# Kernel tuning notes

Hardware: AMD Instinct MI355X
Metric: run time of the kernel (lower is better)

## Reference

```python
import jax, jax.numpy as jnp
import numpy as np

N, E, B, DIM, NF, EF, HID = 50000, 100000, 2000, 64, 14, 4, 128


def setup_inputs() -> dict:
    key = jax.random.key(0)
    ks = jax.random.split(key, 30)
    rn = lambda k, shape, scale: jax.random.normal(k, shape, jnp.float32) * scale
    inp = {}
    inp["x"] = rn(ks[0], (N, NF), 1.0)
    inp["edge_attr"] = jax.random.uniform(ks[1], (E, EF), jnp.float32)
    inp["edge_index"] = jax.random.randint(ks[2], (2, E), 0, N)
    # equal-size graphs: 25 nodes per graph, sorted segment ids
    inp["batch"] = (jnp.arange(N, dtype=jnp.int32) // (N // B)).astype(jnp.int32)
    inp["lin0_w"] = rn(ks[3], (DIM, NF), (1.0 / NF) ** 0.5)
    inp["lin0_b"] = jnp.zeros((DIM,), jnp.float32)
    inp["mlp_w1"] = rn(ks[4], (HID, EF), (1.0 / EF) ** 0.5)
    inp["mlp_b1"] = jnp.zeros((HID,), jnp.float32)
    inp["mlp_w2"] = rn(ks[5], (DIM * DIM, HID), (1.0 / HID) ** 0.5)
    inp["mlp_b2"] = jnp.zeros((DIM * DIM,), jnp.float32)
    inp["root"] = rn(ks[6], (DIM, DIM), (1.0 / DIM) ** 0.5)
    inp["conv_b"] = jnp.zeros((DIM,), jnp.float32)
    inp["gru_wih"] = rn(ks[7], (3 * DIM, DIM), (1.0 / DIM) ** 0.5)
    inp["gru_whh"] = rn(ks[8], (3 * DIM, DIM), (1.0 / DIM) ** 0.5)
    inp["gru_bih"] = jnp.zeros((3 * DIM,), jnp.float32)
    inp["gru_bhh"] = jnp.zeros((3 * DIM,), jnp.float32)
    inp["lstm_wih"] = rn(ks[9], (4 * DIM, 2 * DIM), (1.0 / (2 * DIM)) ** 0.5)
    inp["lstm_whh"] = rn(ks[10], (4 * DIM, DIM), (1.0 / DIM) ** 0.5)
    inp["lstm_bih"] = jnp.zeros((4 * DIM,), jnp.float32)
    inp["lstm_bhh"] = jnp.zeros((4 * DIM,), jnp.float32)
    inp["lin1_w"] = rn(ks[11], (DIM, 2 * DIM), (1.0 / (2 * DIM)) ** 0.5)
    inp["lin1_b"] = jnp.zeros((DIM,), jnp.float32)
    inp["lin2_w"] = rn(ks[12], (1, DIM), (1.0 / DIM) ** 0.5)
    inp["lin2_b"] = jnp.zeros((1,), jnp.float32)
    return inp


def _forward(x, edge_attr, edge_index, batch, lin0_w, lin0_b, mlp_w1, mlp_b1,
             mlp_w2, mlp_b2, root, conv_b, gru_wih, gru_whh, gru_bih, gru_bhh,
             lstm_wih, lstm_whh, lstm_bih, lstm_bhh, lin1_w, lin1_b, lin2_w, lin2_b):
    src, dst = edge_index[0], edge_index[1]
    n = x.shape[0]
    # edge MLP -> per-edge weight matrices [E, DIM, DIM]
    h_e = jax.nn.relu(edge_attr @ mlp_w1.T + mlp_b1)
    W_e = (h_e @ mlp_w2.T + mlp_b2).reshape(-1, DIM, DIM)
    deg = jnp.clip(jax.ops.segment_sum(jnp.ones_like(dst, jnp.float32), dst, n), 1.0)

    out = jax.nn.relu(x @ lin0_w.T + lin0_b)
    h = out  # GRU hidden (seq_len=1, 1 layer)
    for _ in range(3):
        msg = jnp.einsum('ei,eio->eo', out[src], W_e)  # per-edge matmul
        agg = jax.ops.segment_sum(msg, dst, n) / deg[:, None]  # scatter-mean
        m = jax.nn.relu(agg + out @ root + conv_b)  # NNConv: aggr + root + bias
        # GRU step
        gi = m @ gru_wih.T + gru_bih
        gh = h @ gru_whh.T + gru_bhh
        i_r, i_z, i_n = jnp.split(gi, 3, axis=-1)
        h_r, h_z, h_n = jnp.split(gh, 3, axis=-1)
        r = jax.nn.sigmoid(i_r + h_r)
        z = jax.nn.sigmoid(i_z + h_z)
        ng = jnp.tanh(i_n + r * h_n)
        h = (1.0 - z) * ng + z * h
        out = h

    # Set2Set pooling, 3 processing steps
    b = B
    qh = jnp.zeros((b, DIM), out.dtype)
    qc = jnp.zeros((b, DIM), out.dtype)
    q_star = jnp.zeros((b, 2 * DIM), out.dtype)
    for _ in range(3):
        gates = q_star @ lstm_wih.T + lstm_bih + qh @ lstm_whh.T + lstm_bhh
        gi_, gf_, gg_, go_ = jnp.split(gates, 4, axis=-1)
        qc = jax.nn.sigmoid(gf_) * qc + jax.nn.sigmoid(gi_) * jnp.tanh(gg_)
        qh = jax.nn.sigmoid(go_) * jnp.tanh(qc)
        q = qh
        e = jnp.sum(out * q[batch], axis=-1)  # [N]
        e_max = jax.ops.segment_max(e, batch, b)
        a = jnp.exp(e - e_max[batch])
        denom = jax.ops.segment_sum(a, batch, b)
        a = a / denom[batch]
        r_read = jax.ops.segment_sum(a[:, None] * out, batch, b)
        q_star = jnp.concatenate([q, r_read], axis=-1)

    y = jax.nn.relu(q_star @ lin1_w.T + lin1_b)
    y = y @ lin2_w.T + lin2_b
    return y.reshape(-1)


def reference(x, edge_attr, edge_index, batch, lin0_w, lin0_b, mlp_w1, mlp_b1,
              mlp_w2, mlp_b2, root, conv_b, gru_wih, gru_whh, gru_bih, gru_bhh,
              lstm_wih, lstm_whh, lstm_bih, lstm_bhh, lin1_w, lin1_b, lin2_w, lin2_b):
    return _forward(x, edge_attr, edge_index, batch, lin0_w, lin0_b, mlp_w1, mlp_b1,
                    mlp_w2, mlp_b2, root, conv_b, gru_wih, gru_whh, gru_bih, gru_bhh,
                    lstm_wih, lstm_whh, lstm_bih, lstm_bhh, lin1_w, lin1_b, lin2_w, lin2_b)
```

## Files before the change

### kernel.cpp

```cpp
#include <hip/hip_runtime.h>
#include <hip/hip_bf16.h>

#define NN 50000
#define EE 100000
#define BB 2000
#define DIM 64
#define NF 14
#define EF 4
#define HID 128
#define EPAD 100096
#define EPAD2 100352

typedef __attribute__((ext_vector_type(8))) _Float16 half8;
typedef __attribute__((ext_vector_type(4))) _Float16 half4;
typedef __attribute__((ext_vector_type(4))) float floatx4;

__device__ __forceinline__ float rcp_fast(float x) { return __builtin_amdgcn_rcpf(x); }
__device__ __forceinline__ float sig_fast(float x) { return rcp_fast(1.f + __expf(-x)); }
__device__ __forceinline__ float tanh_fast(float x) {
    float e = __expf(2.f * x);
    return 1.f - 2.f * rcp_fast(e + 1.f);
}

__global__ void prep_fused_kernel(
    const float* __restrict__ x, const float* __restrict__ lin0_w,
    const float* __restrict__ lin0_b, float* __restrict__ hv,
    const float* __restrict__ ea, const float* __restrict__ w1,
    const float* __restrict__ b1, _Float16* __restrict__ he,
    const int* __restrict__ ei, float* __restrict__ deg,
    const float* __restrict__ w2, _Float16* __restrict__ W2rT,
    const float* __restrict__ lih, const float* __restrict__ lhh,
    const float* __restrict__ l1, float* __restrict__ lihT,
    float* __restrict__ lhhT, float* __restrict__ l1T,
    const float* __restrict__ root, const float* __restrict__ b2,
    const float* __restrict__ gwih, const float* __restrict__ gwhh,
    const float* __restrict__ gbih, const float* __restrict__ gbhh,
    _Float16* __restrict__ W1h, _Float16* __restrict__ W2h,
    float* __restrict__ fbias) {
    int t = blockIdx.x * 256 + threadIdx.x;

    {
        int el = t >> 4, hc = t & 15;
        if (el < EPAD2) {
            half8 o8 = {0, 0, 0, 0, 0, 0, 0, 0};
            if (el < EE) {
                const float4 a = *(const float4*)(ea + (size_t)el * 4);
                #pragma unroll
                for (int j = 0; j < 8; j++) {
                    int h = hc * 8 + j;
                    const float4 w = *(const float4*)(w1 + h * 4);
                    float acc = fmaxf(b1[h] + a.x * w.x + a.y * w.y + a.z * w.z + a.w * w.w, 0.f);
                    o8[j] = (_Float16)acc;
                }
                if (hc == 0) atomicAdd(&deg[ei[EE + el]], 1.0f);
            }
            *(half8*)(he + (size_t)el * 128 + hc * 8) = o8;
        }
    }
    if (t < NN * 8) {
        int n = t >> 3, dc = t & 7;
        float xv[NF];
        #pragma unroll
        for (int f = 0; f < NF; f++) xv[f] = x[(size_t)n * NF + f];
        float o[8];
        #pragma unroll
        for (int j = 0; j < 8; j++) {
            int d = dc * 8 + j;
            float acc = lin0_b[d];
            #pragma unroll
            for (int f = 0; f < NF; f++) acc += xv[f] * lin0_w[d * NF + f];
            o[j] = fmaxf(acc, 0.f);
        }
        *(float4*)(hv + (size_t)n * 64 + dc * 8)     = make_float4(o[0], o[1], o[2], o[3]);
        *(float4*)(hv + (size_t)n * 64 + dc * 8 + 4) = make_float4(o[4], o[5], o[6], o[7]);
    }
    if (t < 64 * 1024) {
        int o = t >> 10, kc = t & 1023;
        int k0 = kc * 8, i = k0 >> 7, h0 = k0 & 127;
        const float* src = w2 + (size_t)(i * 64 + o) * 128 + h0;
        const float4 a = *(const float4*)src;
        const float4 b = *(const float4*)(src + 4);
        half8 r = {(_Float16)a.x, (_Float16)a.y, (_Float16)a.z, (_Float16)a.w,
                   (_Float16)b.x, (_Float16)b.y, (_Float16)b.z, (_Float16)b.w};
        *(half8*)(W2rT + (size_t)o * 8192 + k0) = r;
    }
    if (t < 256 * 128) { int j = t / 128, k = t % 128; lihT[k * 256 + j] = lih[t]; }
    if (t < 256 * 64) { int j = t / 64, k = t % 64; lhhT[k * 256 + j] = lhh[t]; }
    if (t < 64 * 128) { int d = t / 128, k = t % 128; l1T[k * 64 + d] = l1[t]; }
    if (t < 64 * 128) {
        int n = t >> 7, k = t & 127;
        W1h[t] = (_Float16)(k < 64 ? root[k * 64 + n] : b2[(size_t)(k - 64) * 64 + n]);
    }
    if (t < 256 * 128) {
        int n2 = t >> 7, k = t & 127;
        int g = n2 >> 6, j = n2 & 63;
        float v;
        if (g == 0)      v = (k < 64) ? gwih[j * 64 + k]         : gwhh[j * 64 + (k - 64)];
        else if (g == 1) v = (k < 64) ? gwih[(64 + j) * 64 + k]  : gwhh[(64 + j) * 64 + (k - 64)];
        else if (g == 2) v = (k < 64) ? gwih[(128 + j) * 64 + k] : 0.f;
        else             v = (k < 64) ? 0.f                      : gwhh[(128 + j) * 64 + (k - 64)];
        W2h[t] = (_Float16)v;
    }
    if (t < 256) {
        int g = t >> 6, j = t & 63;
        float v = (g == 0) ? gbih[j] + gbhh[j]
                : (g == 1) ? gbih[64 + j] + gbhh[64 + j]
                : (g == 2) ? gbih[128 + j] : gbhh[128 + j];
        fbias[t] = v;
    }
}

__global__ __launch_bounds__(256, 2) void msg_gemm_kernel(
    const float* __restrict__ hv, const _Float16* __restrict__ he16,
    const _Float16* __restrict__ W2rT, const int* __restrict__ ei,
    float* __restrict__ agg, float* __restrict__ xsum) {
    __shared__ _Float16 sB[2][16 * 64 * 8];
    __shared__ _Float16 sXs[256 * 68];
    __shared__ int sDst[256];
    const int t = threadIdx.x;
    const int eb = blockIdx.x * 256;
    const int lane = t & 63;
    const int w = t >> 6;
    const int col = lane & 15;
    const int quad = lane >> 4;

    if (t < 256) {
        int e = eb + t;
        sDst[t] = (e < EE) ? ei[EE + e] : 0;
    }
    #pragma unroll 4
    for (int rep = 0; rep < 16; rep++) {
        int idx = rep * 256 + t;
        int el = idx >> 4, d4 = idx & 15;
        int e = eb + el;
        float4 v = {0.f, 0.f, 0.f, 0.f};
        if (e < EE) {
            int src = ei[e];
            v = *(const float4*)(hv + (size_t)src * 64 + d4 * 4);
        }
        half4 h4 = {(_Float16)v.x, (_Float16)v.y, (_Float16)v.z, (_Float16)v.w};
        *(half4*)&sXs[el * 68 + d4 * 4] = h4;
    }

    half8 heReg[4][4];
    #pragma unroll
    for (int mt = 0; mt < 4; mt++) {
        int row = eb + w * 64 + mt * 16 + col;
        #pragma unroll
        for (int p = 0; p < 4; p++)
            heReg[mt][p] = *(const half8*)(he16 + (size_t)row * 128 + p * 32 + quad * 8);
    }

    floatx4 Cacc[4][4];
    #pragma unroll
    for (int mt = 0; mt < 4; mt++)
        #pragma unroll
        for (int nt = 0; nt < 4; nt++)
            Cacc[mt][nt] = (floatx4){0.f, 0.f, 0.f, 0.f};

    const size_t gbase = (size_t)(w * 16 + col) * 8192 + quad * 8;
    half8 pre[4];
    {
        #pragma unroll
        for (int rep = 0; rep < 4; rep++)
            pre[rep] = *(const half8*)(W2rT + gbase + 0 * 128 + rep * 32);
        #pragma unroll
        for (int rep = 0; rep < 4; rep++)
            *(half8*)&sB[0][((w * 4 + rep) * 64 + lane) * 8] = pre[rep];
    }
    __syncthreads();

    #pragma unroll 1
    for (int i = 0; i < 64; i++) {
        int buf = i & 1;
        if (i < 63) {
            #pragma unroll
            for (int rep = 0; rep < 4; rep++)
                pre[rep] = *(const half8*)(W2rT + gbase + (size_t)(i + 1) * 128 + rep * 32);
        }
        _Float16 xsx[4];
        #pragma unroll
        for (int mt = 0; mt < 4; mt++)
            xsx[mt] = sXs[(w * 64 + mt * 16 + col) * 68 + i];
        #pragma unroll
        for (int ks = 0; ks < 4; ks++) {
            half8 bfr[4];
            #pragma unroll
            for (int nt = 0; nt < 4; nt++)
                bfr[nt] = *(const half8*)&sB[buf][((nt * 4 + ks) * 64 + lane) * 8];
            #pragma unroll
            for (int mt = 0; mt < 4; mt++) {
                half8 afr = heReg[mt][ks] * xsx[mt];
                #pragma unroll
                for (int nt = 0; nt < 4; nt++)
                    Cacc[mt][nt] = __builtin_amdgcn_mfma_f32_16x16x32_f16(afr, bfr[nt], Cacc[mt][nt], 0, 0, 0);
            }
        }
        if (i < 63) {
            #pragma unroll
            for (int rep = 0; rep < 4; rep++)
                *(half8*)&sB[buf ^ 1][((w * 4 + rep) * 64 + lane) * 8] = pre[rep];
        }
        __syncthreads();
    }

    #pragma unroll
    for (int mt = 0; mt < 4; mt++) {
        #pragma unroll
        for (int r = 0; r < 4; r++) {
            int el = w * 64 + mt * 16 + quad * 4 + r;
            if (eb + el < EE) {
                float* ap = agg + (size_t)sDst[el] * 64 + col;
                #pragma unroll
                for (int nt = 0; nt < 4; nt++)
                    atomicAdd(ap + nt * 16, Cacc[mt][nt][r]);
            }
        }
    }
    #pragma unroll 4
    for (int rep = 0; rep < 64; rep++) {
        int idx = rep * 256 + t;
        int el = idx >> 6, d = idx & 63;
        if (eb + el < EE)
            atomicAdd(&xsum[(size_t)sDst[el] * 64 + d], (float)sXs[el * 68 + d]);
    }
}

__global__ __launch_bounds__(256, 1) void msg_gemm2_kernel(
    const float* __restrict__ hv, const _Float16* __restrict__ he16,
    const _Float16* __restrict__ W2rT, const int* __restrict__ ei,
    float* __restrict__ agg, float* __restrict__ xsum) {
    __shared__ _Float16 sB[2][16 * 64 * 8];
    __shared__ _Float16 sXs[512 * 68];
    __shared__ int sDst[512];
    const int t = threadIdx.x;
    const int eb = blockIdx.x * 512;
    const int lane = t & 63;
    const int w = t >> 6;
    const int col = lane & 15;
    const int quad = lane >> 4;

    #pragma unroll
    for (int rep = 0; rep < 2; rep++) {
        int idx = rep * 256 + t;
        int e = eb + idx;
        sDst[idx] = (e < EE) ? ei[EE + e] : 0;
    }
    #pragma unroll 4
    for (int rep = 0; rep < 32; rep++) {
        int idx = rep * 256 + t;
        int el = idx >> 4, d4 = idx & 15;
        int e = eb + el;
        float4 v = {0.f, 0.f, 0.f, 0.f};
        if (e < EE) {
            int src = ei[e];
            v = *(const float4*)(hv + (size_t)src * 64 + d4 * 4);
        }
        half4 h4 = {(_Float16)v.x, (_Float16)v.y, (_Float16)v.z, (_Float16)v.w};
        *(half4*)&sXs[el * 68 + d4 * 4] = h4;
    }

    half8 heReg[8][4];
    #pragma unroll
    for (int mt = 0; mt < 8; mt++) {
        int row = eb + w * 128 + mt * 16 + col;
        #pragma unroll
        for (int p = 0; p < 4; p++)
            heReg[mt][p] = *(const half8*)(he16 + (size_t)row * 128 + p * 32 + quad * 8);
    }

    floatx4 Cacc[8][4];
    #pragma unroll
    for (int mt = 0; mt < 8; mt++)
        #pragma unroll
        for (int nt = 0; nt < 4; nt++)
            Cacc[mt][nt] = (floatx4){0.f, 0.f, 0.f, 0.f};

    const size_t gbase = (size_t)(w * 16 + col) * 8192 + quad * 8;
    half8 pre[4];
    {
        #pragma unroll
        for (int rep = 0; rep < 4; rep++)
            pre[rep] = *(const half8*)(W2rT + gbase + 0 * 128 + rep * 32);
        #pragma unroll
        for (int rep = 0; rep < 4; rep++)
            *(half8*)&sB[0][((w * 4 + rep) * 64 + lane) * 8] = pre[rep];
    }
    __syncthreads();

    #pragma unroll 1
    for (int i = 0; i < 64; i++) {
        int buf = i & 1;
        if (i < 63) {
            #pragma unroll
            for (int rep = 0; rep < 4; rep++)
                pre[rep] = *(const half8*)(W2rT + gbase + (size_t)(i + 1) * 128 + rep * 32);
        }
        _Float16 xsx[8];
        #pragma unroll
        for (int mt = 0; mt < 8; mt++)
            xsx[mt] = sXs[(w * 128 + mt * 16 + col) * 68 + i];
        #pragma unroll
        for (int ks = 0; ks < 4; ks++) {
            half8 bfr[4];
            #pragma unroll
            for (int nt = 0; nt < 4; nt++)
                bfr[nt] = *(const half8*)&sB[buf][((nt * 4 + ks) * 64 + lane) * 8];
            #pragma unroll
            for (int mt = 0; mt < 8; mt++) {
                half8 afr = heReg[mt][ks] * xsx[mt];
                #pragma unroll
                for (int nt = 0; nt < 4; nt++)
                    Cacc[mt][nt] = __builtin_amdgcn_mfma_f32_16x16x32_f16(afr, bfr[nt], Cacc[mt][nt], 0, 0, 0);
            }
        }
        if (i < 63) {
            #pragma unroll
            for (int rep = 0; rep < 4; rep++)
                *(half8*)&sB[buf ^ 1][((w * 4 + rep) * 64 + lane) * 8] = pre[rep];
        }
        __syncthreads();
    }

    #pragma unroll
    for (int mt = 0; mt < 8; mt++) {
        #pragma unroll
        for (int r = 0; r < 4; r++) {
            int el = w * 128 + mt * 16 + quad * 4 + r;
            if (eb + el < EE) {
                float* ap = agg + (size_t)sDst[el] * 64 + col;
                #pragma unroll
                for (int nt = 0; nt < 4; nt++)
                    atomicAdd(ap + nt * 16, Cacc[mt][nt][r]);
            }
        }
    }
    #pragma unroll 4
    for (int rep = 0; rep < 128; rep++) {
        int idx = rep * 256 + t;
        int el = idx >> 6, d = idx & 63;
        if (eb + el < EE)
            atomicAdd(&xsum[(size_t)sDst[el] * 64 + d], (float)sXs[el * 68 + d]);
    }
}

__global__ __launch_bounds__(256, 2) void node_fused_kernel(
    const float* __restrict__ hv_in, float* __restrict__ agg,
    float* __restrict__ xsum, const float* __restrict__ deg,
    const _Float16* __restrict__ W1h, const _Float16* __restrict__ W2h,
    const float* __restrict__ fbias, const float* __restrict__ cb,
    float* __restrict__ hv_out) {
    __shared__ _Float16 sA1[64 * 136];
    __shared__ _Float16 sA2[64 * 136];
    __shared__ float sH[64 * 68];
    __shared__ float sAgg[64 * 68];
    const int t = threadIdx.x;
    const int nb = blockIdx.x * 64;
    const int n = t >> 2, part = t & 3;
    {
        int gn = nb + n;
        bool valid = gn < NN;
        float inv = 1.f;
        if (valid) inv = 1.f / fmaxf(deg[gn], 1.f);
        #pragma unroll
        for (int c4 = 0; c4 < 4; c4++) {
            int d0 = part * 16 + c4 * 4;
            float4 hvv = {0.f, 0.f, 0.f, 0.f}, agv = {0.f, 0.f, 0.f, 0.f}, xsv = {0.f, 0.f, 0.f, 0.f};
            if (valid) {
                hvv = *(const float4*)(hv_in + (size_t)gn * 64 + d0);
                agv = *(const float4*)(agg + (size_t)gn * 64 + d0);
                xsv = *(const float4*)(xsum + (size_t)gn * 64 + d0);
            }
            agv.x *= inv; agv.y *= inv; agv.z *= inv; agv.w *= inv;
            xsv.x *= inv; xsv.y *= inv; xsv.z *= inv; xsv.w *= inv;
            half4 hvh = {(_Float16)hvv.x, (_Float16)hvv.y, (_Float16)hvv.z, (_Float16)hvv.w};
            half4 xsh = {(_Float16)xsv.x, (_Float16)xsv.y, (_Float16)xsv.z, (_Float16)xsv.w};
            *(half4*)&sA1[n * 136 + d0] = hvh;
            *(half4*)&sA1[n * 136 + 64 + d0] = xsh;
            *(half4*)&sA2[n * 136 + 64 + d0] = hvh;
            *(float4*)&sH[n * 68 + d0] = hvv;
            *(float4*)&sAgg[n * 68 + d0] = agv;
        }
        if (valid) {
            float4 z = {0.f, 0.f, 0.f, 0.f};
            #pragma unroll
            for (int c4 = 0; c4 < 4; c4++) {
                int d0 = part * 16 + c4 * 4;
                *(float4*)(agg + (size_t)gn * 64 + d0) = z;
                *(float4*)(xsum + (size_t)gn * 64 + d0) = z;
            }
        }
    }
    __syncthreads();

    const int lane = t & 63, w = t >> 6;
    const int col = lane & 15, quad = lane >> 4;

    floatx4 C1[4];
    #pragma unroll
    for (int nt = 0; nt < 4; nt++) {
        float b = cb[nt * 16 + col];
        C1[nt] = (floatx4){b, b, b, b};
    }
    #pragma unroll
    for (int ks = 0; ks < 4; ks++) {
        half8 a = *(const half8*)&sA1[(w * 16 + col) * 136 + ks * 32 + quad * 8];
        #pragma unroll
        for (int nt = 0; nt < 4; nt++) {
            half8 bfr = *(const half8*)(W1h + (size_t)(nt * 16 + col) * 128 + ks * 32 + quad * 8);
            C1[nt] = __builtin_amdgcn_mfma_f32_16x16x32_f16(a, bfr, C1[nt], 0, 0, 0);
        }
    }
    #pragma unroll
    for (int nt = 0; nt < 4; nt++) {
        #pragma unroll
        for (int r = 0; r < 4; r++) {
            int node = w * 16 + quad * 4 + r;
            int j = nt * 16 + col;
            float m = fmaxf(C1[nt][r] + sAgg[node * 68 + j], 0.f);
            sA2[node * 136 + j] = (_Float16)m;
        }
    }
    __syncthreads();

    floatx4 C2[16];
    #pragma unroll
    for (int nt2 = 0; nt2 < 16; nt2++) {
        float b = fbias[nt2 * 16 + col];
        C2[nt2] = (floatx4){b, b, b, b};
    }
    #pragma unroll
    for (int ks = 0; ks < 4; ks++) {
        half8 a = *(const half8*)&sA2[(w * 16 + col) * 136 + ks * 32 + quad * 8];
        #pragma unroll
        for (int nt2 = 0; nt2 < 16; nt2++) {
            half8 bfr = *(const half8*)(W2h + (size_t)(nt2 * 16 + col) * 128 + ks * 32 + quad * 8);
            C2[nt2] = __builtin_amdgcn_mfma_f32_16x16x32_f16(a, bfr, C2[nt2], 0, 0, 0);
        }
    }
    float hnew[4][4];
    #pragma unroll
    for (int r = 0; r < 4; r++) {
        int node = w * 16 + quad * 4 + r;
        #pragma unroll
        for (int jt = 0; jt < 4; jt++) {
            int j = jt * 16 + col;
            float rr = sig_fast(C2[jt][r]);
            float zz = sig_fast(C2[4 + jt][r]);
            float ng = tanh_fast(C2[8 + jt][r] + rr * C2[12 + jt][r]);
            float hold = sH[node * 68 + j];
            hnew[r][jt] = (1.f - zz) * ng + zz * hold;
        }
    }
    __syncthreads();
    #pragma unroll
    for (int r = 0; r < 4; r++) {
        int node = w * 16 + quad * 4 + r;
        #pragma unroll
        for (int jt = 0; jt < 4; jt++)
            sH[node * 68 + jt * 16 + col] = hnew[r][jt];
    }
    __syncthreads();
    {
        int gn = nb + n;
        if (gn < NN) {
            #pragma unroll
            for (int c4 = 0; c4 < 4; c4++) {
                int d0 = part * 16 + c4 * 4;
                *(float4*)(hv_out + (size_t)gn * 64 + d0) = *(const float4*)&sH[n * 68 + d0];
            }
        }
    }
}

__global__ __launch_bounds__(256) void set2set_kernel(
    const float* __restrict__ hv,
    const float* __restrict__ lihT, const float* __restrict__ lhhT,
    const float* __restrict__ l_bih, const float* __restrict__ l_bhh,
    const float* __restrict__ lin1T, const float* __restrict__ lin1_b,
    const float* __restrict__ lin2_w, const float* __restrict__ lin2_b,
    float* __restrict__ out) {
    __shared__ float outS[25 * 65];
    __shared__ float qs[128], qh[64], qc[64], gat[256], ew[32], aw[32], red[64];
    int g = blockIdx.x;
    int t = threadIdx.x;
    for (int p = t; p < 25 * 64; p += 256) {
        int j = p >> 6, i = p & 63;
        outS[j * 65 + i] = hv[(size_t)(g * 25 + j) * 64 + i];
    }
    if (t < 128) qs[t] = 0.f;
    if (t < 64) { qh[t] = 0.f; qc[t] = 0.f; }
    __syncthreads();
    for (int it = 0; it < 3; it++) {
        float acc = l_bih[t] + l_bhh[t];
        for (int k = 0; k < 128; k++) acc += qs[k] * lihT[k * 256 + t];
        for (int k = 0; k < 64; k++) acc += qh[k] * lhhT[k * 256 + t];
        gat[t] = acc;
        __syncthreads();
        if (t < 64) {
            float ig = sig_fast(gat[t]);
            float fg = sig_fast(gat[64 + t]);
            float gg = tanh_fast(gat[128 + t]);
            float og = sig_fast(gat[192 + t]);
            float c = fg * qc[t] + ig * gg;
            qc[t] = c;
            qh[t] = og * tanh_fast(c);
        }
        __syncthreads();
        if (t < 25) {
            float e = 0.f;
            for (int i = 0; i < 64; i++) e += outS[t * 65 + i] * qh[i];
            ew[t] = e;
        }
        __syncthreads();
        if (t == 0) {
            float mx = ew[0];
            for (int j = 1; j < 25; j++) mx = fmaxf(mx, ew[j]);
            float s = 0.f;
            for (int j = 0; j < 25; j++) { float a = __expf(ew[j] - mx); aw[j] = a; s += a; }
            float inv = rcp_fast(s);
            for (int j = 0; j < 25; j++) aw[j] *= inv;
        }
        __syncthreads();
        if (t < 64) {
            float r = 0.f;
            for (int j = 0; j < 25; j++) r += aw[j] * outS[j * 65 + t];
            qs[t] = qh[t];
            qs[64 + t] = r;
        }
        __syncthreads();
    }
    if (t < 64) {
        float y1 = lin1_b[t];
        for (int k = 0; k < 128; k++) y1 += qs[k] * lin1T[k * 64 + t];
        y1 = fmaxf(y1, 0.f);
        red[t] = y1 * lin2_w[t];
    }
    __syncthreads();
    if (t == 0) {
        float y = lin2_b[0];
        for (int i = 0; i < 64; i++) y += red[i];
        out[g] = y;
    }
}

extern "C" void kernel_launch(void* const* d_in, const int* in_sizes, int n_in,
                              void* d_out, int out_size, void* d_ws, size_t ws_size,
                              hipStream_t stream) {
    const float* x        = (const float*)d_in[0];
    const float* ea       = (const float*)d_in[1];
    const int*   ei       = (const int*)  d_in[2];
    const float* lin0_w   = (const float*)d_in[4];
    const float* lin0_b   = (const float*)d_in[5];
    const float* mlp_w1   = (const float*)d_in[6];
    const float* mlp_b1   = (const float*)d_in[7];
    const float* mlp_w2   = (const float*)d_in[8];
    const float* mlp_b2   = (const float*)d_in[9];
    const float* root     = (const float*)d_in[10];
    const float* conv_b   = (const float*)d_in[11];
    const float* gru_wih  = (const float*)d_in[12];
    const float* gru_whh  = (const float*)d_in[13];
    const float* gru_bih  = (const float*)d_in[14];
    const float* gru_bhh  = (const float*)d_in[15];
    const float* lstm_wih = (const float*)d_in[16];
    const float* lstm_whh = (const float*)d_in[17];
    const float* lstm_bih = (const float*)d_in[18];
    const float* lstm_bhh = (const float*)d_in[19];
    const float* lin1_w   = (const float*)d_in[20];
    const float* lin1_b   = (const float*)d_in[21];
    const float* lin2_w   = (const float*)d_in[22];
    const float* lin2_b   = (const float*)d_in[23];
    float* out = (float*)d_out;

    char* base = (char*)d_ws;
    size_t off = 0;
    auto carve = [&](size_t bytes) -> void* {
        void* r = base + off;
        off = (off + bytes + 255) & ~(size_t)255;
        return r;
    };
    float* hv   = (float*)carve((size_t)NN * 64 * 4);
    float* agg  = (float*)carve((size_t)NN * 64 * 4);
    float* xsum = (float*)carve((size_t)NN * 64 * 4);
    float* deg  = (float*)carve((size_t)NN * 4);
    float* lihT = (float*)carve(128 * 256 * 4);
    float* lhhT = (float*)carve(64 * 256 * 4);
    float* l1T  = (float*)carve(128 * 64 * 4);
    float* fbias = (float*)carve(256 * 4);
    _Float16* he16 = (_Float16*)carve((size_t)EPAD2 * 128 * 2);
    _Float16* W2rT = (_Float16*)carve((size_t)64 * 8192 * 2);
    _Float16* W1h  = (_Float16*)carve((size_t)64 * 128 * 2);
    _Float16* W2h  = (_Float16*)carve((size_t)256 * 128 * 2);

    hipMemsetAsync(agg, 0, (size_t)NN * 64 * 4 * 2 + (size_t)NN * 4, stream);
    prep_fused_kernel<<<EPAD2 * 16 / 256, 256, 0, stream>>>(
        x, lin0_w, lin0_b, hv,
        ea, mlp_w1, mlp_b1, he16, ei, deg,
        mlp_w2, W2rT,
        lstm_wih, lstm_whh, lin1_w, lihT, lhhT, l1T,
        root, mlp_b2, gru_wih, gru_whh, gru_bih, gru_bhh,
        W1h, W2h, fbias);

    for (int it = 0; it < 3; it++) {
        if (it == 0)
            msg_gemm2_kernel<<<EPAD2 / 512, 256, 0, stream>>>(hv, he16, W2rT, ei, agg, xsum);
        else
            msg_gemm_kernel<<<EPAD / 256, 256, 0, stream>>>(hv, he16, W2rT, ei, agg, xsum);
        node_fused_kernel<<<(NN + 63) / 64, 256, 0, stream>>>(hv, agg, xsum, deg,
                                                              W1h, W2h, fbias, conv_b, hv);
    }

    set2set_kernel<<<BB, 256, 0, stream>>>(hv, lihT, lhhT, lstm_bih, lstm_bhh,
                                           l1T, lin1_b, lin2_w, lin2_b, out);
}
```

Before: 768.5 us.

## Shrink first message GEMM blocks, drop node shared buffer, parallelize softmax

The first-iteration message GEMM moves from 256-thread blocks over 512 edges to 128-thread blocks over 128 edges. This roughly quadruples the grid and halves per-wave accumulators, at the cost of more W2rT reloads per edge. The node kernel drops its sH shared buffer, reads old hidden values from global memory into registers, and writes GRU outputs directly, removing two barriers so it can target 3 blocks per SM. The set2set softmax now uses a 32-lane shuffle reduction instead of a single serial thread.

```diff
diff --git a/kernel.cpp b/kernel.cpp
--- a/kernel.cpp
+++ b/kernel.cpp
@@ -226,29 +226,27 @@
     }
 }
 
-__global__ __launch_bounds__(256, 1) void msg_gemm2_kernel(
+__global__ __launch_bounds__(128, 2) void msg_gemm2_kernel(
     const float* __restrict__ hv, const _Float16* __restrict__ he16,
     const _Float16* __restrict__ W2rT, const int* __restrict__ ei,
     float* __restrict__ agg, float* __restrict__ xsum) {
     __shared__ _Float16 sB[2][16 * 64 * 8];
-    __shared__ _Float16 sXs[512 * 68];
-    __shared__ int sDst[512];
+    __shared__ _Float16 sXs[128 * 68];
+    __shared__ int sDst[128];
     const int t = threadIdx.x;
-    const int eb = blockIdx.x * 512;
+    const int eb = blockIdx.x * 128;
     const int lane = t & 63;
     const int w = t >> 6;
     const int col = lane & 15;
     const int quad = lane >> 4;
 
-    #pragma unroll
-    for (int rep = 0; rep < 2; rep++) {
-        int idx = rep * 256 + t;
-        int e = eb + idx;
-        sDst[idx] = (e < EE) ? ei[EE + e] : 0;
+    if (t < 128) {
+        int e = eb + t;
+        sDst[t] = (e < EE) ? ei[EE + e] : 0;
     }
     #pragma unroll 4
-    for (int rep = 0; rep < 32; rep++) {
-        int idx = rep * 256 + t;
+    for (int rep = 0; rep < 16; rep++) {
+        int idx = rep * 128 + t;
         int el = idx >> 4, d4 = idx & 15;
         int e = eb + el;
         float4 v = {0.f, 0.f, 0.f, 0.f};
@@ -260,31 +258,37 @@
         *(half4*)&sXs[el * 68 + d4 * 4] = h4;
     }
 
-    half8 heReg[8][4];
-    #pragma unroll
-    for (int mt = 0; mt < 8; mt++) {
-        int row = eb + w * 128 + mt * 16 + col;
+    half8 heReg[4][4];
+    #pragma unroll
+    for (int mt = 0; mt < 4; mt++) {
+        int row = eb + w * 64 + mt * 16 + col;
         #pragma unroll
         for (int p = 0; p < 4; p++)
             heReg[mt][p] = *(const half8*)(he16 + (size_t)row * 128 + p * 32 + quad * 8);
     }
 
-    floatx4 Cacc[8][4];
-    #pragma unroll
-    for (int mt = 0; mt < 8; mt++)
+    floatx4 Cacc[4][4];
+    #pragma unroll
+    for (int mt = 0; mt < 4; mt++)
         #pragma unroll
         for (int nt = 0; nt < 4; nt++)
             Cacc[mt][nt] = (floatx4){0.f, 0.f, 0.f, 0.f};
 
-    const size_t gbase = (size_t)(w * 16 + col) * 8192 + quad * 8;
-    half8 pre[4];
+    size_t goff[8]; int woff[8];
+    #pragma unroll
+    for (int rep = 0; rep < 8; rep++) {
+        int f = w * 8 + rep;
+        goff[rep] = (size_t)((f >> 2) * 16 + col) * 8192 + (f & 3) * 32 + quad * 8;
+        woff[rep] = (f * 64 + lane) * 8;
+    }
+    half8 pre[8];
     {
         #pragma unroll
-        for (int rep = 0; rep < 4; rep++)
-            pre[rep] = *(const half8*)(W2rT + gbase + 0 * 128 + rep * 32);
-        #pragma unroll
-        for (int rep = 0; rep < 4; rep++)
-            *(half8*)&sB[0][((w * 4 + rep) * 64 + lane) * 8] = pre[rep];
+        for (int rep = 0; rep < 8; rep++)
+            pre[rep] = *(const half8*)(W2rT + goff[rep]);
+        #pragma unroll
+        for (int rep = 0; rep < 8; rep++)
+            *(half8*)&sB[0][woff[rep]] = pre[rep];
     }
     __syncthreads();
 
@@ -293,13 +297,13 @@
         int buf = i & 1;
         if (i < 63) {
             #pragma unroll
-            for (int rep = 0; rep < 4; rep++)
-                pre[rep] = *(const half8*)(W2rT + gbase + (size_t)(i + 1) * 128 + rep * 32);
-        }
-        _Float16 xsx[8];
-        #pragma unroll
-        for (int mt = 0; mt < 8; mt++)
-            xsx[mt] = sXs[(w * 128 + mt * 16 + col) * 68 + i];
+            for (int rep = 0; rep < 8; rep++)
+                pre[rep] = *(const half8*)(W2rT + goff[rep] + (size_t)(i + 1) * 128);
+        }
+        _Float16 xsx[4];
+        #pragma unroll
+        for (int mt = 0; mt < 4; mt++)
+            xsx[mt] = sXs[(w * 64 + mt * 16 + col) * 68 + i];
         #pragma unroll
         for (int ks = 0; ks < 4; ks++) {
             half8 bfr[4];
@@ -307,7 +311,7 @@
             for (int nt = 0; nt < 4; nt++)
                 bfr[nt] = *(const half8*)&sB[buf][((nt * 4 + ks) * 64 + lane) * 8];
             #pragma unroll
-            for (int mt = 0; mt < 8; mt++) {
+            for (int mt = 0; mt < 4; mt++) {
                 half8 afr = heReg[mt][ks] * xsx[mt];
                 #pragma unroll
                 for (int nt = 0; nt < 4; nt++)
@@ -316,17 +320,17 @@
         }
         if (i < 63) {
             #pragma unroll
-            for (int rep = 0; rep < 4; rep++)
-                *(half8*)&sB[buf ^ 1][((w * 4 + rep) * 64 + lane) * 8] = pre[rep];
+            for (int rep = 0; rep < 8; rep++)
+                *(half8*)&sB[buf ^ 1][woff[rep]] = pre[rep];
         }
         __syncthreads();
     }
 
     #pragma unroll
-    for (int mt = 0; mt < 8; mt++) {
+    for (int mt = 0; mt < 4; mt++) {
         #pragma unroll
         for (int r = 0; r < 4; r++) {
-            int el = w * 128 + mt * 16 + quad * 4 + r;
+            int el = w * 64 + mt * 16 + quad * 4 + r;
             if (eb + el < EE) {
                 float* ap = agg + (size_t)sDst[el] * 64 + col;
                 #pragma unroll
@@ -336,15 +340,15 @@
         }
     }
     #pragma unroll 4
-    for (int rep = 0; rep < 128; rep++) {
-        int idx = rep * 256 + t;
+    for (int rep = 0; rep < 64; rep++) {
+        int idx = rep * 128 + t;
         int el = idx >> 6, d = idx & 63;
         if (eb + el < EE)
             atomicAdd(&xsum[(size_t)sDst[el] * 64 + d], (float)sXs[el * 68 + d]);
     }
 }
 
-__global__ __launch_bounds__(256, 2) void node_fused_kernel(
+__global__ __launch_bounds__(256, 3) void node_fused_kernel(
     const float* __restrict__ hv_in, float* __restrict__ agg,
     float* __restrict__ xsum, const float* __restrict__ deg,
     const _Float16* __restrict__ W1h, const _Float16* __restrict__ W2h,
@@ -352,7 +356,6 @@
     float* __restrict__ hv_out) {
     __shared__ _Float16 sA1[64 * 136];
     __shared__ _Float16 sA2[64 * 136];
-    __shared__ float sH[64 * 68];
     __shared__ float sAgg[64 * 68];
     const int t = threadIdx.x;
     const int nb = blockIdx.x * 64;
@@ -378,7 +381,6 @@
             *(half4*)&sA1[n * 136 + d0] = hvh;
             *(half4*)&sA1[n * 136 + 64 + d0] = xsh;
             *(half4*)&sA2[n * 136 + 64 + d0] = hvh;
-            *(float4*)&sH[n * 68 + d0] = hvv;
             *(float4*)&sAgg[n * 68 + d0] = agv;
         }
         if (valid) {
@@ -423,6 +425,16 @@
     }
     __syncthreads();
 
+    float holdv[4][4];
+    #pragma unroll
+    for (int r = 0; r < 4; r++) {
+        int node = w * 16 + quad * 4 + r;
+        int gn2 = nb + node;
+        #pragma unroll
+        for (int jt = 0; jt < 4; jt++)
+            holdv[r][jt] = (gn2 < NN) ? hv_in[(size_t)gn2 * 64 + jt * 16 + col] : 0.f;
+    }
+
     floatx4 C2[16];
     #pragma unroll
     for (int nt2 = 0; nt2 < 16; nt2++) {
@@ -438,36 +450,18 @@
             C2[nt2] = __builtin_amdgcn_mfma_f32_16x16x32_f16(a, bfr, C2[nt2], 0, 0, 0);
         }
     }
-    float hnew[4][4];
     #pragma unroll
     for (int r = 0; r < 4; r++) {
         int node = w * 16 + quad * 4 + r;
-        #pragma unroll
-        for (int jt = 0; jt < 4; jt++) {
-            int j = jt * 16 + col;
-            float rr = sig_fast(C2[jt][r]);
-            float zz = sig_fast(C2[4 + jt][r]);
-            float ng = tanh_fast(C2[8 + jt][r] + rr * C2[12 + jt][r]);
-            float hold = sH[node * 68 + j];
-            hnew[r][jt] = (1.f - zz) * ng + zz * hold;
-        }
-    }
-    __syncthreads();
-    #pragma unroll
-    for (int r = 0; r < 4; r++) {
-        int node = w * 16 + quad * 4 + r;
-        #pragma unroll
-        for (int jt = 0; jt < 4; jt++)
-            sH[node * 68 + jt * 16 + col] = hnew[r][jt];
-    }
-    __syncthreads();
-    {
-        int gn = nb + n;
-        if (gn < NN) {
-            #pragma unroll
-            for (int c4 = 0; c4 < 4; c4++) {
-                int d0 = part * 16 + c4 * 4;
-                *(float4*)(hv_out + (size_t)gn * 64 + d0) = *(const float4*)&sH[n * 68 + d0];
+        int gn2 = nb + node;
+        if (gn2 < NN) {
+            #pragma unroll
+            for (int jt = 0; jt < 4; jt++) {
+                int j = jt * 16 + col;
+                float rr = sig_fast(C2[jt][r]);
+                float zz = sig_fast(C2[4 + jt][r]);
+                float ng = tanh_fast(C2[8 + jt][r] + rr * C2[12 + jt][r]);
+                hv_out[(size_t)gn2 * 64 + j] = (1.f - zz) * ng + zz * holdv[r][jt];
             }
         }
     }
@@ -513,13 +507,16 @@
             ew[t] = e;
         }
         __syncthreads();
-        if (t == 0) {
-            float mx = ew[0];
-            for (int j = 1; j < 25; j++) mx = fmaxf(mx, ew[j]);
-            float s = 0.f;
-            for (int j = 0; j < 25; j++) { float a = __expf(ew[j] - mx); aw[j] = a; s += a; }
-            float inv = rcp_fast(s);
-            for (int j = 0; j < 25; j++) aw[j] *= inv;
+        if (t < 32) {
+            float e = (t < 25) ? ew[t] : -1e30f;
+            float mx = e;
+            #pragma unroll
+            for (int o = 16; o > 0; o >>= 1) mx = fmaxf(mx, __shfl_xor(mx, o, 32));
+            float a = (t < 25) ? __expf(e - mx) : 0.f;
+            float s = a;
+            #pragma unroll
+            for (int o = 16; o > 0; o >>= 1) s += __shfl_xor(s, o, 32);
+            if (t < 25) aw[t] = a * rcp_fast(s);
         }
         __syncthreads();
         if (t < 64) {
@@ -603,7 +600,7 @@
 
     for (int it = 0; it < 3; it++) {
         if (it == 0)
-            msg_gemm2_kernel<<<EPAD2 / 512, 256, 0, stream>>>(hv, he16, W2rT, ei, agg, xsum);
+            msg_gemm2_kernel<<<EPAD / 128, 128, 0, stream>>>(hv, he16, W2rT, ei, agg, xsum);
         else
             msg_gemm_kernel<<<EPAD / 256, 256, 0, stream>>>(hv, he16, W2rT, ei, agg, xsum);
         node_fused_kernel<<<(NN + 63) / 64, 256, 0, stream>>>(hv, agg, xsum, deg,
```

New measurement: 829.3 us. 7.9% more time.
